# Kernel optimization log

Hardware: AMD Instinct MI355X
Metric: run time of the kernel (lower is better)

The kernel has to match this reference:

```python
import jax, jax.numpy as jnp
from jax import lax
import numpy as np

N_VOX = 50000
B = 2
D, H, W = 8, 160, 160
CIN = 16
G = 3
K = 27
CHANS = [(16, 16), (16, 32), (32, 64), (64, 64), (64, 128)]
NAMES = ['in', 'e1', 'e2', 'e3', 'out']


def setup_inputs() -> dict:
    key = jax.random.key(0)
    ks = jax.random.split(key, 16)
    rng = np.random.default_rng(0)
    # unique active cells -> deterministic scatter/gather rulebook
    lin = rng.choice(B * D * H * W, size=N_VOX, replace=False)
    bz = lin // (D * H * W)
    rem = lin % (D * H * W)
    zz = rem // (H * W)
    yy = (rem % (H * W)) // W
    xx = rem % W
    coors = jnp.asarray(np.stack([bz, zz, yy, xx], 1).astype(np.int32))
    inp = {
        'voxel_features': jax.random.normal(ks[0], (N_VOX, CIN), jnp.float32),
        'coors': coors,
        'batch_size': B,
    }
    i = 1
    for nm, (ci, co) in zip(NAMES, CHANS):
        k1, k2 = jax.random.split(ks[i]); i += 1
        inp['wb_' + nm] = jax.random.normal(k1, (K, ci, co), jnp.float32) * 0.05
        inp['ws_' + nm] = jax.random.normal(k2, (K, ci, G, co), jnp.float32) * 0.05
        inp['gm_' + nm] = jnp.ones((co,), jnp.float32)
        inp['bt_' + nm] = jnp.zeros((co,), jnp.float32)
    return inp


def _kan_block(feat, nbr, wb, ws, gm, bt, centers, inv_h):
    # submanifold KAN conv: gather -> (silu base + RBF spline basis) GEMM -> accumulate
    n = feat.shape[0]
    fp = jnp.concatenate([feat, jnp.zeros((1, feat.shape[1]), feat.dtype)], 0)  # pad row for out-of-grid

    def body(acc, kin):
        idx, wbk, wsk = kin
        x = fp[idx]                                   # [N, Cin] gathered neighbors
        base = jax.nn.silu(x) @ wbk                   # [N, Cout]
        bas = jnp.exp(-jnp.square((x[:, :, None] - centers) * inv_h))  # [N, Cin, G]
        spl = jnp.einsum('ncg,cgo->no', bas, wsk)     # [N, Cout]
        return acc + base + spl, None

    out0 = jnp.zeros((n, wb.shape[-1]), feat.dtype)
    out, _ = lax.scan(jax.checkpoint(body), out0, (nbr, wb, ws))
    # BatchNorm1d (train-mode batch stats) + ReLU
    mu = out.mean(0)
    var = out.var(0)
    out = (out - mu) * lax.rsqrt(var + 1e-3) * gm + bt
    return jax.nn.relu(out)


def _build_rulebook(coors, batch_size, n):
    grid = jnp.full((batch_size, D + 2, H + 2, W + 2), n, jnp.int32)
    grid = grid.at[coors[:, 0], coors[:, 1] + 1, coors[:, 2] + 1, coors[:, 3] + 1].set(
        jnp.arange(n, dtype=jnp.int32))
    offs = [(dz, dy, dx) for dz in (-1, 0, 1) for dy in (-1, 0, 1) for dx in (-1, 0, 1)]
    return jnp.stack([
        grid[coors[:, 0], coors[:, 1] + 1 + dz, coors[:, 2] + 1 + dy, coors[:, 3] + 1 + dx]
        for dz, dy, dx in offs])  # [27, N]


def reference(voxel_features, coors, batch_size,
              wb_in, ws_in, gm_in, bt_in,
              wb_e1, ws_e1, gm_e1, bt_e1,
              wb_e2, ws_e2, gm_e2, bt_e2,
              wb_e3, ws_e3, gm_e3, bt_e3,
              wb_out, ws_out, gm_out, bt_out):
    n = voxel_features.shape[0]
    nbr = _build_rulebook(coors, batch_size, n)
    centers = jnp.linspace(-1.0, 1.0, G)
    inv_h = (G - 1) / 2.0
    x = _kan_block(voxel_features, nbr, wb_in, ws_in, gm_in, bt_in, centers, inv_h)
    x = _kan_block(x, nbr, wb_e1, ws_e1, gm_e1, bt_e1, centers, inv_h)
    x = _kan_block(x, nbr, wb_e2, ws_e2, gm_e2, bt_e2, centers, inv_h)
    x = _kan_block(x, nbr, wb_e3, ws_e3, gm_e3, bt_e3, centers, inv_h)
    x = _kan_block(x, nbr, wb_out, ws_out, gm_out, bt_out, centers, inv_h)
    co = x.shape[1]
    dense = jnp.zeros((batch_size, D, H, W, co), x.dtype)
    dense = dense.at[coors[:, 0], coors[:, 1], coors[:, 2], coors[:, 3]].set(x)
    dense = dense.transpose(0, 4, 1, 2, 3)            # [B, C, D, H, W]
    return dense.reshape(batch_size, co * D, H, W)    # [B, C*D, H, W]
```

## Files before the change

### kernel.cpp

```cpp
#include <hip/hip_runtime.h>

#define N_VOX 50000
#define BATCH 2
#define DD 8
#define HH 160
#define WW 160
#define PD 10
#define PH 162
#define PW 162
#define KK 27
#define NCELL (BATCH*DD*HH*WW)
#define GRID_ELEMS (BATCH*PD*PH*PW)
#define OUT_ELEMS (BATCH*128*DD*HH*WW)

typedef __attribute__((ext_vector_type(8))) short short8v;
typedef __attribute__((ext_vector_type(4))) float float4v;

__device__ inline unsigned short f2bf(float f) {
    unsigned u = __float_as_uint(f);
    u += 0x7FFFu + ((u >> 16) & 1u);
    return (unsigned short)(u >> 16);
}

__global__ void k_flags(const int* __restrict__ coors, int* __restrict__ flags) {
    int n = blockIdx.x * 256 + threadIdx.x;
    if (n >= N_VOX) return;
    int b = coors[n*4+0], z = coors[n*4+1], y = coors[n*4+2], x = coors[n*4+3];
    flags[((b*DD + z)*HH + y)*WW + x] = 1;
}

__global__ void k_scan1(const int* __restrict__ flags, int* __restrict__ scanout,
                        int* __restrict__ bsums) {
    __shared__ int s[256];
    int t = threadIdx.x, blk = blockIdx.x;
    int4 v = ((const int4*)(flags + blk*1024))[t];
    int tsum = v.x + v.y + v.z + v.w;
    s[t] = tsum; __syncthreads();
    for (int off = 1; off < 256; off <<= 1) {
        int x = (t >= off) ? s[t-off] : 0;
        __syncthreads(); s[t] += x; __syncthreads();
    }
    int excl = s[t] - tsum;
    int4 o; o.x = excl; o.y = excl + v.x; o.z = o.y + v.y; o.w = o.z + v.z;
    ((int4*)(scanout + blk*1024))[t] = o;
    if (t == 255) bsums[blk] = s[255];
}

__global__ void k_scan2(int* __restrict__ bsums) {
    __shared__ int s[512];
    int t = threadIdx.x;
    int orig = (t < 400) ? bsums[t] : 0;
    s[t] = orig; __syncthreads();
    for (int off = 1; off < 512; off <<= 1) {
        int x = (t >= off) ? s[t-off] : 0;
        __syncthreads(); s[t] += x; __syncthreads();
    }
    if (t < 400) bsums[t] = s[t] - orig;
}

__global__ void k_pos(const int* __restrict__ coors, const int* __restrict__ scanout,
                      const int* __restrict__ bsums, int* __restrict__ pos_of,
                      int* __restrict__ vox_at) {
    int n = blockIdx.x * 256 + threadIdx.x;
    if (n >= N_VOX) return;
    int b = coors[n*4+0], z = coors[n*4+1], y = coors[n*4+2], x = coors[n*4+3];
    int lin = ((b*DD + z)*HH + y)*WW + x;
    int pos = scanout[lin] + bsums[lin >> 10];
    pos_of[n] = pos;
    vox_at[pos] = n;
}

__global__ void k_gridP(const int* __restrict__ coors, const int* __restrict__ pos_of,
                        int* __restrict__ gridP) {
    int n = blockIdx.x * 256 + threadIdx.x;
    if (n >= N_VOX) return;
    int b = coors[n*4+0], z = coors[n*4+1], y = coors[n*4+2], x = coors[n*4+3];
    gridP[((b*PD + z+1)*PH + (y+1))*PW + (x+1)] = pos_of[n];
}

__global__ void k_nbrP(const int* __restrict__ coors, const int* __restrict__ vox_at,
                       const int* __restrict__ gridP, int* __restrict__ nbrP) {
    int i = blockIdx.x * 256 + threadIdx.x;
    if (i >= N_VOX) return;
    int n = vox_at[i];
    int b = coors[n*4+0], z = coors[n*4+1]+1, y = coors[n*4+2]+1, x = coors[n*4+3]+1;
    int k = 0;
    for (int dz = -1; dz <= 1; ++dz)
        for (int dy = -1; dy <= 1; ++dy)
            for (int dx = -1; dx <= 1; ++dx) {
                int g = gridP[((b*PD + z+dz)*PH + (y+dy))*PW + (x+dx)];
                nbrP[k*N_VOX + i] = (g >= 0) ? g : N_VOX;
                ++k;
            }
}

__global__ void k_phi0(const float* __restrict__ vf, const int* __restrict__ vox_at,
                       unsigned short* __restrict__ phi) {
    int e = blockIdx.x * 256 + threadIdx.x;
    if (e >= (N_VOX + 1) * 16) return;
    int i = e / 16, c = e % 16;
    float x = 0.f;
    if (i < N_VOX) x = vf[(size_t)vox_at[i] * 16 + c];
    float sig = 1.f / (1.f + __expf(-x));
    ushort4 p;
    p.x = f2bf(x * sig);
    p.y = f2bf(__expf(-(x + 1.f) * (x + 1.f)));
    p.z = f2bf(__expf(-x * x));
    p.w = f2bf(__expf(-(x - 1.f) * (x - 1.f)));
    *(ushort4*)&phi[(size_t)e * 4] = p;
}

struct WswzArgs {
    const float* wb[5];
    const float* ws[5];
    unsigned short* dst[5];
};
__global__ void k_wswz_all(WswzArgs a) {
    constexpr int off[6]   = {0, 27648, 82944, 304128, 746496, 1631232};
    constexpr int lgCI4[5] = {6, 6, 7, 8, 8};
    constexpr int lgCO[5]  = {4, 5, 6, 6, 7};
    int e = blockIdx.x * 256 + threadIdx.x;
    if (e >= off[5]) return;
    int L = 0;
    #pragma unroll
    for (int i = 1; i < 5; ++i) L += (e >= off[i]);
    int el = e - off[L];
    int CIN4 = 1 << lgCI4[L], COUT = 1 << lgCO[L], CIN = CIN4 >> 2;
    int j8   = el & 7;
    int rest = el >> 3;
    int o    = rest & (COUT - 1);
    int kb   = rest >> lgCO[L];
    int kabs = kb * 8 + j8;
    int k  = kabs >> lgCI4[L];
    int c4 = kabs & (CIN4 - 1);
    int c = c4 >> 2, jj = c4 & 3;
    float v = (jj == 0) ? a.wb[L][(k * CIN + c) * COUT + o]
                        : a.ws[L][((k * CIN + c) * 3 + (jj - 1)) * COUT + o];
    a.dst[L][el] = f2bf(v);
}

template<int CIN, int COUT, int NSPL>
__global__ __launch_bounds__(256) void k_conv_mfma(
    const unsigned short* __restrict__ phi,
    const int*            __restrict__ nbrP,
    const unsigned short* __restrict__ Wsw,
    float*                __restrict__ pre,
    float*                __restrict__ sums)
{
    constexpr int CIN4   = CIN * 4;
    constexpr int BK     = 64;
    constexpr int SPK    = CIN4 / BK;
    constexpr int NSTAGE = KK * SPK;
    constexpr int COUTH  = COUT / NSPL;
    constexpr int NFW    = COUTH / 16;
    constexpr int NMB    = (N_VOX + 127) / 128;
    constexpr int NBLK   = NMB * NSPL;
    constexpr int PERX   = (NBLK + 7) / 8;

    int lb = blockIdx.x;
    int linear = (lb & 7) * PERX + (lb >> 3);
    if (linear >= NBLK) return;
    const int mb = linear / NSPL, h = linear % NSPL;

    const int t = threadIdx.x, lane = t & 63, wv = t >> 6;
    const int l15 = lane & 15, q = lane >> 4;
    const int base = mb * 128;
    const int vg0 = base + wv * 32 + l15, vg1 = vg0 + 16;
    const int ob = h * COUTH;

    const unsigned short* bp = Wsw + (size_t)(q * COUT + ob + l15) * 8;

    int rows[2], rowsN[2];
    short8v A0[2][2], A1[2][2];
    short8v B0[2][NFW], B1[2][NFW];

    auto loadB = [&](int sp, short8v (&Bb)[2][NFW]) {
        #pragma unroll
        for (int kk = 0; kk < 2; ++kk)
            #pragma unroll
            for (int nf = 0; nf < NFW; ++nf)
                Bb[kk][nf] = *(const short8v*)(bp +
                    ((size_t)(sp * 8 + kk * 4) * COUT + nf * 16) * 8);
    };
    auto loadA = [&](int sp, short8v (&Ab)[2][2]) {
        if (sp % SPK == 0) { rows[0] = rowsN[0]; rows[1] = rowsN[1]; }
        const int c4s = (sp % SPK) * BK;
        const unsigned short* p0 = phi + (size_t)rows[0] * CIN4 + c4s + q * 8;
        const unsigned short* p1 = phi + (size_t)rows[1] * CIN4 + c4s + q * 8;
        Ab[0][0] = *(const short8v*)p0;        Ab[0][1] = *(const short8v*)p1;
        Ab[1][0] = *(const short8v*)(p0 + 32); Ab[1][1] = *(const short8v*)(p1 + 32);
        if (sp % SPK == 0) {
            int k2 = sp / SPK + 1;
            if (k2 < KK) {
                rowsN[0] = (vg0 < N_VOX) ? nbrP[k2 * N_VOX + vg0] : N_VOX;
                rowsN[1] = (vg1 < N_VOX) ? nbrP[k2 * N_VOX + vg1] : N_VOX;
            }
        }
    };

    float4v acc[2][NFW];
    #pragma unroll
    for (int mi = 0; mi < 2; ++mi)
        #pragma unroll
        for (int nf = 0; nf < NFW; ++nf)
            acc[mi][nf] = (float4v){0.f, 0.f, 0.f, 0.f};

    auto domfma = [&](const short8v (&Ab)[2][2], const short8v (&Bb)[2][NFW]) {
        #pragma unroll
        for (int kk = 0; kk < 2; ++kk)
            #pragma unroll
            for (int nf = 0; nf < NFW; ++nf) {
                acc[0][nf] = __builtin_amdgcn_mfma_f32_16x16x32_bf16(Ab[kk][0], Bb[kk][nf], acc[0][nf], 0, 0, 0);
                acc[1][nf] = __builtin_amdgcn_mfma_f32_16x16x32_bf16(Ab[kk][1], Bb[kk][nf], acc[1][nf], 0, 0, 0);
            }
    };

    rows[0]  = (vg0 < N_VOX) ? nbrP[vg0] : N_VOX;
    rows[1]  = (vg1 < N_VOX) ? nbrP[vg1] : N_VOX;
    rowsN[0] = (vg0 < N_VOX) ? nbrP[N_VOX + vg0] : N_VOX;
    rowsN[1] = (vg1 < N_VOX) ? nbrP[N_VOX + vg1] : N_VOX;
    loadB(0, B0);
    {
        const unsigned short* p0 = phi + (size_t)rows[0] * CIN4 + q * 8;
        const unsigned short* p1 = phi + (size_t)rows[1] * CIN4 + q * 8;
        A0[0][0] = *(const short8v*)p0;        A0[0][1] = *(const short8v*)p1;
        A0[1][0] = *(const short8v*)(p0 + 32); A0[1][1] = *(const short8v*)(p1 + 32);
    }

    int s = 0;
    for (; s + 2 <= NSTAGE; s += 2) {
        loadB(s + 1, B1); loadA(s + 1, A1);
        __builtin_amdgcn_sched_barrier(0);
        domfma(A0, B0);
        if (s + 2 < NSTAGE) { loadB(s + 2, B0); loadA(s + 2, A0); }
        __builtin_amdgcn_sched_barrier(0);
        domfma(A1, B1);
    }
    if (s < NSTAGE) domfma(A0, B0);

    #pragma unroll
    for (int mi = 0; mi < 2; ++mi)
        #pragma unroll
        for (int nf = 0; nf < NFW; ++nf)
            #pragma unroll
            for (int r = 0; r < 4; ++r) {
                int v = base + wv * 32 + mi * 16 + q * 4 + r;
                if (v < N_VOX)
                    pre[(size_t)v * COUT + ob + nf * 16 + l15] = acc[mi][nf][r];
            }

    float* S = sums + (blockIdx.x & 7) * 256;
    #pragma unroll
    for (int nf = 0; nf < NFW; ++nf) {
        float s1 = 0.f, s2 = 0.f;
        #pragma unroll
        for (int mi = 0; mi < 2; ++mi)
            #pragma unroll
            for (int r = 0; r < 4; ++r) {
                int v = base + wv * 32 + mi * 16 + q * 4 + r;
                if (v < N_VOX) {
                    float a = acc[mi][nf][r];
                    s1 += a; s2 += a * a;
                }
            }
        s1 += __shfl_xor(s1, 16); s1 += __shfl_xor(s1, 32);
        s2 += __shfl_xor(s2, 16); s2 += __shfl_xor(s2, 32);
        if (q == 0) {
            atomicAdd(&S[ob + nf * 16 + l15], s1);
            atomicAdd(&S[COUT + ob + nf * 16 + l15], s2);
        }
    }
}

template<int COUT>
__global__ void k_bnapply_phi(const float* __restrict__ pre, const float* __restrict__ sums,
                              const float* __restrict__ gm, const float* __restrict__ bt,
                              unsigned short* __restrict__ phi) {
    __shared__ float sc[COUT], sh[COUT];
    int t = threadIdx.x;
    if (t < COUT) {
        float s1 = 0.f, s2 = 0.f;
        #pragma unroll
        for (int xo = 0; xo < 8; ++xo) {
            s1 += sums[xo * 256 + t];
            s2 += sums[xo * 256 + COUT + t];
        }
        float mu  = s1 * (1.f / N_VOX);
        float var = s2 * (1.f / N_VOX) - mu*mu;
        float s = rsqrtf(var + 1e-3f) * gm[t];
        sc[t] = s;
        sh[t] = bt[t] - mu * s;
    }
    __syncthreads();
    int tot = (N_VOX + 1) * COUT;
    for (int e = blockIdx.x*256 + t; e < tot; e += gridDim.x*256) {
        int i = e / COUT, c = e % COUT;
        float x = 0.f;
        if (i < N_VOX) x = fmaxf(pre[(size_t)i*COUT + c] * sc[c] + sh[c], 0.f);
        float sig = 1.f / (1.f + __expf(-x));
        ushort4 p;
        p.x = f2bf(x * sig);
        p.y = f2bf(__expf(-(x + 1.f) * (x + 1.f)));
        p.z = f2bf(__expf(-x * x));
        p.w = f2bf(__expf(-(x - 1.f) * (x - 1.f)));
        *(ushort4*)&phi[(size_t)e * 4] = p;
    }
}

template<int COUT>
__global__ void k_bnapply_f32(float* __restrict__ pre, const float* __restrict__ sums,
                              const float* __restrict__ gm, const float* __restrict__ bt) {
    __shared__ float sc[COUT], sh[COUT];
    int t = threadIdx.x;
    if (t < COUT) {
        float s1 = 0.f, s2 = 0.f;
        #pragma unroll
        for (int xo = 0; xo < 8; ++xo) {
            s1 += sums[xo * 256 + t];
            s2 += sums[xo * 256 + COUT + t];
        }
        float mu  = s1 * (1.f / N_VOX);
        float var = s2 * (1.f / N_VOX) - mu*mu;
        float s = rsqrtf(var + 1e-3f) * gm[t];
        sc[t] = s;
        sh[t] = bt[t] - mu * s;
    }
    __syncthreads();
    for (int e = blockIdx.x*256 + t; e < N_VOX*COUT; e += gridDim.x*256) {
        int c = e % COUT;
        pre[e] = fmaxf(pre[e] * sc[c] + sh[c], 0.f);
    }
}

__global__ void k_dense(const float* __restrict__ feat, const int* __restrict__ gridP,
                        float* __restrict__ out) {
    int e4 = blockIdx.x*256 + threadIdx.x;
    if (e4 >= OUT_ELEMS/4) return;
    int e = e4 * 4;
    int x  = e % WW;
    int y  = (e / WW) % HH;
    int cz = (e / (WW*HH)) % (128*DD);
    int b  = e / (WW*HH*128*DD);
    int c = cz >> 3, z = cz & 7;
    const int* gp = &gridP[((b*PD + z+1)*PH + (y+1))*PW + (x+1)];
    int g0 = gp[0], g1 = gp[1], g2 = gp[2], g3 = gp[3];
    float4 o;
    o.x = (g0 >= 0) ? feat[(size_t)g0*128 + c] : 0.f;
    o.y = (g1 >= 0) ? feat[(size_t)g1*128 + c] : 0.f;
    o.z = (g2 >= 0) ? feat[(size_t)g2*128 + c] : 0.f;
    o.w = (g3 >= 0) ? feat[(size_t)g3*128 + c] : 0.f;
    *(float4*)&out[e] = o;
}

template<int CIN, int COUT, int NSPL>
static void run_block(const float* gm, const float* bt,
                      const int* nbrP, unsigned short* phi, const unsigned short* Wsw,
                      float* sums, float* pre, bool last, hipStream_t stream) {
    constexpr int NMB  = (N_VOX + 127) / 128;
    constexpr int NBLK = NMB * NSPL;
    constexpr int GRID = ((NBLK + 7) / 8) * 8;
    k_conv_mfma<CIN, COUT, NSPL><<<GRID, 256, 0, stream>>>(phi, nbrP, Wsw, pre, sums);
    if (last) {
        k_bnapply_f32<COUT><<<512, 256, 0, stream>>>(pre, sums, gm, bt);
    } else {
        k_bnapply_phi<COUT><<<512, 256, 0, stream>>>(pre, sums, gm, bt, phi);
    }
}

extern "C" void kernel_launch(void* const* d_in, const int* in_sizes, int n_in,
                              void* d_out, int out_size, void* d_ws, size_t ws_size,
                              hipStream_t stream) {
    const float* vf    = (const float*)d_in[0];
    const int*   coors = (const int*)d_in[1];
    const float* wb[5] = {(const float*)d_in[3],  (const float*)d_in[7],
                          (const float*)d_in[11], (const float*)d_in[15],
                          (const float*)d_in[19]};
    const float* wsp[5]= {(const float*)d_in[4],  (const float*)d_in[8],
                          (const float*)d_in[12], (const float*)d_in[16],
                          (const float*)d_in[20]};
    const float* gm[5] = {(const float*)d_in[5],  (const float*)d_in[9],
                          (const float*)d_in[13], (const float*)d_in[17],
                          (const float*)d_in[21]};
    const float* bt[5] = {(const float*)d_in[6],  (const float*)d_in[10],
                          (const float*)d_in[14], (const float*)d_in[18],
                          (const float*)d_in[22]};

    char* p = (char*)d_ws;
    auto alloc = [&](size_t bytes) {
        char* r = p;
        p += (bytes + 255) & ~(size_t)255;
        return r;
    };
    int*            flags   = (int*)           alloc((size_t)NCELL * 4);
    int*            scanout = (int*)           alloc((size_t)NCELL * 4);
    int*            bsums   = (int*)           alloc(512 * 4);
    int*            pos_of  = (int*)           alloc((size_t)N_VOX * 4);
    int*            vox_at  = (int*)           alloc((size_t)N_VOX * 4);
    int*            gridP   = (int*)           alloc((size_t)GRID_ELEMS * 4);
    int*            nbrP    = (int*)           alloc((size_t)KK * N_VOX * 4);
    unsigned short* Wsw0    = (unsigned short*)alloc((size_t)KK * 64  * 16  * 2);
    unsigned short* Wsw1    = (unsigned short*)alloc((size_t)KK * 64  * 32  * 2);
    unsigned short* Wsw2    = (unsigned short*)alloc((size_t)KK * 128 * 64  * 2);
    unsigned short* Wsw3    = (unsigned short*)alloc((size_t)KK * 256 * 64  * 2);
    unsigned short* Wsw4    = (unsigned short*)alloc((size_t)KK * 256 * 128 * 2);
    unsigned short* phi     = (unsigned short*)alloc((size_t)(N_VOX + 1) * 256 * 2);
    float*          sumsAll = (float*)         alloc(5 * 8 * 256 * 4);
    float*          pre     = (float*)         alloc((size_t)N_VOX * 128 * 4);

    hipMemsetAsync(flags, 0, (size_t)NCELL * 4, stream);
    hipMemsetAsync(gridP, 0xFF, (size_t)GRID_ELEMS * 4, stream);
    hipMemsetAsync(sumsAll, 0, 5 * 8 * 256 * 4, stream);

    WswzArgs wa;
    for (int i = 0; i < 5; ++i) { wa.wb[i] = wb[i]; wa.ws[i] = wsp[i]; }
    wa.dst[0] = Wsw0; wa.dst[1] = Wsw1; wa.dst[2] = Wsw2; wa.dst[3] = Wsw3; wa.dst[4] = Wsw4;
    k_wswz_all<<<(1631232 + 255) / 256, 256, 0, stream>>>(wa);

    k_flags<<<(N_VOX+255)/256, 256, 0, stream>>>(coors, flags);
    k_scan1<<<NCELL/1024, 256, 0, stream>>>(flags, scanout, bsums);
    k_scan2<<<1, 512, 0, stream>>>(bsums);
    k_pos  <<<(N_VOX+255)/256, 256, 0, stream>>>(coors, scanout, bsums, pos_of, vox_at);
    k_gridP<<<(N_VOX+255)/256, 256, 0, stream>>>(coors, pos_of, gridP);
    k_nbrP <<<(N_VOX+255)/256, 256, 0, stream>>>(coors, vox_at, gridP, nbrP);
    {
        int n = (N_VOX + 1) * 16;
        k_phi0<<<(n + 255) / 256, 256, 0, stream>>>(vf, vox_at, phi);
    }

    run_block<16, 16,  1>(gm[0], bt[0], nbrP, phi, Wsw0, sumsAll + 0*2048, pre, false, stream);
    run_block<16, 32,  1>(gm[1], bt[1], nbrP, phi, Wsw1, sumsAll + 1*2048, pre, false, stream);
    run_block<32, 64,  1>(gm[2], bt[2], nbrP, phi, Wsw2, sumsAll + 2*2048, pre, false, stream);
    run_block<64, 64,  1>(gm[3], bt[3], nbrP, phi, Wsw3, sumsAll + 3*2048, pre, false, stream);
    run_block<64, 128, 2>(gm[4], bt[4], nbrP, phi, Wsw4, sumsAll + 4*2048, pre, true,  stream);

    k_dense<<<(OUT_ELEMS/4 + 255)/256, 256, 0, stream>>>(pre, gridP, (float*)d_out);
}
```

Baseline: 737.9 us.

## Use 32x32x16 bf16 MFMA for conv layers with COUT>=32

Adds a conv kernel built on the 32x32x16 bf16 MFMA. It is used for layers 1-4, while layer 0 (COUT=16) keeps the 16x16 variant. The weight swizzle kernel now emits a matching 16-element-per-output layout for those layers. The aim is fewer MFMA instructions and better operand reuse per gathered A row, since one wave covers 32 voxels in a single tile. In exchange each lane holds more accumulator registers (16 floats per output tile), which may reduce occupancy.

```diff
diff --git a/kernel.cpp b/kernel.cpp
--- a/kernel.cpp
+++ b/kernel.cpp
@@ -13,8 +13,9 @@
 #define GRID_ELEMS (BATCH*PD*PH*PW)
 #define OUT_ELEMS (BATCH*128*DD*HH*WW)
 
-typedef __attribute__((ext_vector_type(8))) short short8v;
-typedef __attribute__((ext_vector_type(4))) float float4v;
+typedef __attribute__((ext_vector_type(8)))  short short8v;
+typedef __attribute__((ext_vector_type(4)))  float float4v;
+typedef __attribute__((ext_vector_type(16))) float float16v;
 
 __device__ inline unsigned short f2bf(float f) {
     unsigned u = __float_as_uint(f);
@@ -126,11 +127,20 @@
     for (int i = 1; i < 5; ++i) L += (e >= off[i]);
     int el = e - off[L];
     int CIN4 = 1 << lgCI4[L], COUT = 1 << lgCO[L], CIN = CIN4 >> 2;
-    int j8   = el & 7;
-    int rest = el >> 3;
-    int o    = rest & (COUT - 1);
-    int kb   = rest >> lgCO[L];
-    int kabs = kb * 8 + j8;
+    int kabs, o;
+    if (L == 0) {
+        int j8 = el & 7;
+        int rest = el >> 3;
+        o = rest & (COUT - 1);
+        int kb = rest >> lgCO[L];
+        kabs = kb * 8 + j8;
+    } else {
+        int j = el & 7;
+        int half = (el >> 3) & 1;
+        o = (el >> 4) & (COUT - 1);
+        int kb = el >> (4 + lgCO[L]);
+        kabs = kb * 16 + half * 8 + j;
+    }
     int k  = kabs >> lgCI4[L];
     int c4 = kabs & (CIN4 - 1);
     int c = c4 >> 2, jj = c4 & 3;
@@ -139,36 +149,32 @@
     a.dst[L][el] = f2bf(v);
 }
 
-template<int CIN, int COUT, int NSPL>
-__global__ __launch_bounds__(256) void k_conv_mfma(
-    const unsigned short* __restrict__ phi,
-    const int*            __restrict__ nbrP,
-    const unsigned short* __restrict__ Wsw,
-    float*                __restrict__ pre,
-    float*                __restrict__ sums)
+template<int CIN, int COUT>
+__global__ __launch_bounds__(256) void k_conv_mfma16(
+    const unsigned short* __restrict__ phi, const int* __restrict__ nbrP,
+    const unsigned short* __restrict__ Wsw, float* __restrict__ pre,
+    float* __restrict__ sums)
 {
     constexpr int CIN4   = CIN * 4;
     constexpr int BK     = 64;
     constexpr int SPK    = CIN4 / BK;
     constexpr int NSTAGE = KK * SPK;
-    constexpr int COUTH  = COUT / NSPL;
-    constexpr int NFW    = COUTH / 16;
+    constexpr int NFW    = COUT / 16;
     constexpr int NMB    = (N_VOX + 127) / 128;
-    constexpr int NBLK   = NMB * NSPL;
+    constexpr int NBLK   = NMB;
     constexpr int PERX   = (NBLK + 7) / 8;
 
     int lb = blockIdx.x;
     int linear = (lb & 7) * PERX + (lb >> 3);
     if (linear >= NBLK) return;
-    const int mb = linear / NSPL, h = linear % NSPL;
+    const int mb = linear;
 
     const int t = threadIdx.x, lane = t & 63, wv = t >> 6;
     const int l15 = lane & 15, q = lane >> 4;
     const int base = mb * 128;
     const int vg0 = base + wv * 32 + l15, vg1 = vg0 + 16;
-    const int ob = h * COUTH;
-
-    const unsigned short* bp = Wsw + (size_t)(q * COUT + ob + l15) * 8;
+
+    const unsigned short* bp = Wsw + (size_t)(q * COUT + l15) * 8;
 
     int rows[2], rowsN[2];
     short8v A0[2][2], A1[2][2];
@@ -246,7 +252,7 @@
             for (int r = 0; r < 4; ++r) {
                 int v = base + wv * 32 + mi * 16 + q * 4 + r;
                 if (v < N_VOX)
-                    pre[(size_t)v * COUT + ob + nf * 16 + l15] = acc[mi][nf][r];
+                    pre[(size_t)v * COUT + nf * 16 + l15] = acc[mi][nf][r];
             }
 
     float* S = sums + (blockIdx.x & 7) * 256;
@@ -266,8 +272,131 @@
         s1 += __shfl_xor(s1, 16); s1 += __shfl_xor(s1, 32);
         s2 += __shfl_xor(s2, 16); s2 += __shfl_xor(s2, 32);
         if (q == 0) {
-            atomicAdd(&S[ob + nf * 16 + l15], s1);
-            atomicAdd(&S[COUT + ob + nf * 16 + l15], s2);
+            atomicAdd(&S[nf * 16 + l15], s1);
+            atomicAdd(&S[COUT + nf * 16 + l15], s2);
+        }
+    }
+}
+
+template<int CIN, int COUT, int NSPL>
+__global__ __launch_bounds__(256) void k_conv_mfma32(
+    const unsigned short* __restrict__ phi,
+    const int*            __restrict__ nbrP,
+    const unsigned short* __restrict__ Wsw,
+    float*                __restrict__ pre,
+    float*                __restrict__ sums)
+{
+    constexpr int CIN4   = CIN * 4;
+    constexpr int BK     = 64;
+    constexpr int SPK    = CIN4 / BK;
+    constexpr int NSTAGE = KK * SPK;
+    constexpr int COUTH  = COUT / NSPL;
+    constexpr int NF     = COUTH / 32;
+    constexpr int NMB    = (N_VOX + 127) / 128;
+    constexpr int NBLK   = NMB * NSPL;
+    constexpr int PERX   = (NBLK + 7) / 8;
+
+    int lb = blockIdx.x;
+    int linear = (lb & 7) * PERX + (lb >> 3);
+    if (linear >= NBLK) return;
+    const int mb = linear / NSPL, h = linear % NSPL;
+
+    const int t = threadIdx.x, lane = t & 63, wv = t >> 6;
+    const int l31 = lane & 31, half = lane >> 5;
+    const int base = mb * 128;
+    const int vg = base + wv * 32 + l31;
+    const int ob = h * COUTH;
+
+    const unsigned short* bp = Wsw + (size_t)((ob + l31) * 2 + half) * 8;
+
+    int row, rowN;
+    short8v A0[4], A1[4];
+    short8v B0[4][NF], B1[4][NF];
+
+    auto loadB = [&](int sp, short8v (&Bb)[4][NF]) {
+        #pragma unroll
+        for (int ks = 0; ks < 4; ++ks)
+            #pragma unroll
+            for (int nf = 0; nf < NF; ++nf)
+                Bb[ks][nf] = *(const short8v*)(bp +
+                    (size_t)((sp * 4 + ks) * COUT + nf * 32) * 16);
+    };
+    auto loadA = [&](int sp, short8v (&Ab)[4]) {
+        if (sp % SPK == 0) row = rowN;
+        const int c4s = (sp % SPK) * BK;
+        const unsigned short* p = phi + (size_t)row * CIN4 + c4s + half * 8;
+        #pragma unroll
+        for (int ks = 0; ks < 4; ++ks)
+            Ab[ks] = *(const short8v*)(p + ks * 16);
+        if (sp % SPK == 0) {
+            int k2 = sp / SPK + 1;
+            if (k2 < KK) rowN = (vg < N_VOX) ? nbrP[k2 * N_VOX + vg] : N_VOX;
+        }
+    };
+
+    float16v acc[NF];
+    #pragma unroll
+    for (int nf = 0; nf < NF; ++nf)
+        #pragma unroll
+        for (int r = 0; r < 16; ++r) acc[nf][r] = 0.f;
+
+    auto domfma = [&](const short8v (&Ab)[4], const short8v (&Bb)[4][NF]) {
+        #pragma unroll
+        for (int ks = 0; ks < 4; ++ks)
+            #pragma unroll
+            for (int nf = 0; nf < NF; ++nf)
+                acc[nf] = __builtin_amdgcn_mfma_f32_32x32x16_bf16(Ab[ks], Bb[ks][nf], acc[nf], 0, 0, 0);
+    };
+
+    row  = (vg < N_VOX) ? nbrP[vg] : N_VOX;
+    rowN = (vg < N_VOX) ? nbrP[N_VOX + vg] : N_VOX;
+    loadB(0, B0);
+    {
+        const unsigned short* p = phi + (size_t)row * CIN4 + half * 8;
+        #pragma unroll
+        for (int ks = 0; ks < 4; ++ks)
+            A0[ks] = *(const short8v*)(p + ks * 16);
+    }
+
+    int s = 0;
+    for (; s + 2 <= NSTAGE; s += 2) {
+        loadB(s + 1, B1); loadA(s + 1, A1);
+        __builtin_amdgcn_sched_barrier(0);
+        domfma(A0, B0);
+        if (s + 2 < NSTAGE) { loadB(s + 2, B0); loadA(s + 2, A0); }
+        __builtin_amdgcn_sched_barrier(0);
+        domfma(A1, B1);
+    }
+    if (s < NSTAGE) domfma(A0, B0);
+
+    #pragma unroll
+    for (int nf = 0; nf < NF; ++nf)
+        #pragma unroll
+        for (int r = 0; r < 16; ++r) {
+            int rw = (r & 3) + 8 * (r >> 2) + 4 * half;
+            int v = base + wv * 32 + rw;
+            if (v < N_VOX)
+                pre[(size_t)v * COUT + ob + nf * 32 + l31] = acc[nf][r];
+        }
+
+    float* S = sums + (blockIdx.x & 7) * 256;
+    #pragma unroll
+    for (int nf = 0; nf < NF; ++nf) {
+        float s1 = 0.f, s2 = 0.f;
+        #pragma unroll
+        for (int r = 0; r < 16; ++r) {
+            int rw = (r & 3) + 8 * (r >> 2) + 4 * half;
+            int v = base + wv * 32 + rw;
+            if (v < N_VOX) {
+                float a = acc[nf][r];
+                s1 += a; s2 += a * a;
+            }
+        }
+        s1 += __shfl_xor(s1, 32);
+        s2 += __shfl_xor(s2, 32);
+        if (half == 0) {
+            atomicAdd(&S[ob + nf * 32 + l31], s1);
+            atomicAdd(&S[COUT + ob + nf * 32 + l31], s2);
         }
     }
 }
@@ -353,13 +482,13 @@
 }
 
 template<int CIN, int COUT, int NSPL>
-static void run_block(const float* gm, const float* bt,
-                      const int* nbrP, unsigned short* phi, const unsigned short* Wsw,
-                      float* sums, float* pre, bool last, hipStream_t stream) {
+static void run_block32(const float* gm, const float* bt,
+                        const int* nbrP, unsigned short* phi, const unsigned short* Wsw,
+                        float* sums, float* pre, bool last, hipStream_t stream) {
     constexpr int NMB  = (N_VOX + 127) / 128;
     constexpr int NBLK = NMB * NSPL;
     constexpr int GRID = ((NBLK + 7) / 8) * 8;
-    k_conv_mfma<CIN, COUT, NSPL><<<GRID, 256, 0, stream>>>(phi, nbrP, Wsw, pre, sums);
+    k_conv_mfma32<CIN, COUT, NSPL><<<GRID, 256, 0, stream>>>(phi, nbrP, Wsw, pre, sums);
     if (last) {
         k_bnapply_f32<COUT><<<512, 256, 0, stream>>>(pre, sums, gm, bt);
     } else {
@@ -427,11 +556,17 @@
         k_phi0<<<(n + 255) / 256, 256, 0, stream>>>(vf, vox_at, phi);
     }
 
-    run_block<16, 16,  1>(gm[0], bt[0], nbrP, phi, Wsw0, sumsAll + 0*2048, pre, false, stream);
-    run_block<16, 32,  1>(gm[1], bt[1], nbrP, phi, Wsw1, sumsAll + 1*2048, pre, false, stream);
-    run_block<32, 64,  1>(gm[2], bt[2], nbrP, phi, Wsw2, sumsAll + 2*2048, pre, false, stream);
-    run_block<64, 64,  1>(gm[3], bt[3], nbrP, phi, Wsw3, sumsAll + 3*2048, pre, false, stream);
-    run_block<64, 128, 2>(gm[4], bt[4], nbrP, phi, Wsw4, sumsAll + 4*2048, pre, true,  stream);
+    {
+        constexpr int NMB = (N_VOX + 127) / 128;
+        constexpr int GRID = ((NMB + 7) / 8) * 8;
+        k_conv_mfma16<16, 16><<<GRID, 256, 0, stream>>>(phi, nbrP, Wsw0, pre, sumsAll + 0*2048);
+        k_bnapply_phi<16><<<512, 256, 0, stream>>>(pre, sumsAll + 0*2048, gm[0], bt[0], phi);
+    }
+
+    run_block32<16, 32,  1>(gm[1], bt[1], nbrP, phi, Wsw1, sumsAll + 1*2048, pre, false, stream);
+    run_block32<32, 64,  1>(gm[2], bt[2], nbrP, phi, Wsw2, sumsAll + 2*2048, pre, false, stream);
+    run_block32<64, 64,  1>(gm[3], bt[3], nbrP, phi, Wsw3, sumsAll + 3*2048, pre, false, stream);
+    run_block32<64, 128, 2>(gm[4], bt[4], nbrP, phi, Wsw4, sumsAll + 4*2048, pre, true,  stream);
 
     k_dense<<<(OUT_ELEMS/4 + 255)/256, 256, 0, stream>>>(pre, gridP, (float*)d_out);
 }
```

Result: no change. 750.6 us (+1.7%).

## Stage conv weights through double-buffered LDS shared by all waves

Applied to the files above, without the earlier changes.

Adds a new conv kernel in which the block cooperatively loads weight tiles for groups of three stages into double-buffered shared memory, instead of each wave fetching its B fragments from global memory into registers. The four waves then read B from LDS while the gathered activation rows are still prefetched per stage. The aim is to cut redundant global and L2 weight traffic and register pressure across waves. The cost is a __syncthreads per group and LDS usage that may limit occupancy. The first layer keeps the old register-path kernel, now specialised without the output-channel split.

```diff
diff --git a/kernel.cpp b/kernel.cpp
--- a/kernel.cpp
+++ b/kernel.cpp
@@ -139,36 +139,32 @@
     a.dst[L][el] = f2bf(v);
 }
 
-template<int CIN, int COUT, int NSPL>
-__global__ __launch_bounds__(256) void k_conv_mfma(
-    const unsigned short* __restrict__ phi,
-    const int*            __restrict__ nbrP,
-    const unsigned short* __restrict__ Wsw,
-    float*                __restrict__ pre,
-    float*                __restrict__ sums)
+template<int CIN, int COUT>
+__global__ __launch_bounds__(256) void k_conv_mfma16(
+    const unsigned short* __restrict__ phi, const int* __restrict__ nbrP,
+    const unsigned short* __restrict__ Wsw, float* __restrict__ pre,
+    float* __restrict__ sums)
 {
     constexpr int CIN4   = CIN * 4;
     constexpr int BK     = 64;
     constexpr int SPK    = CIN4 / BK;
     constexpr int NSTAGE = KK * SPK;
-    constexpr int COUTH  = COUT / NSPL;
-    constexpr int NFW    = COUTH / 16;
+    constexpr int NFW    = COUT / 16;
     constexpr int NMB    = (N_VOX + 127) / 128;
-    constexpr int NBLK   = NMB * NSPL;
+    constexpr int NBLK   = NMB;
     constexpr int PERX   = (NBLK + 7) / 8;
 
     int lb = blockIdx.x;
     int linear = (lb & 7) * PERX + (lb >> 3);
     if (linear >= NBLK) return;
-    const int mb = linear / NSPL, h = linear % NSPL;
+    const int mb = linear;
 
     const int t = threadIdx.x, lane = t & 63, wv = t >> 6;
     const int l15 = lane & 15, q = lane >> 4;
     const int base = mb * 128;
     const int vg0 = base + wv * 32 + l15, vg1 = vg0 + 16;
-    const int ob = h * COUTH;
-
-    const unsigned short* bp = Wsw + (size_t)(q * COUT + ob + l15) * 8;
+
+    const unsigned short* bp = Wsw + (size_t)(q * COUT + l15) * 8;
 
     int rows[2], rowsN[2];
     short8v A0[2][2], A1[2][2];
@@ -237,6 +233,157 @@
         domfma(A1, B1);
     }
     if (s < NSTAGE) domfma(A0, B0);
+
+    #pragma unroll
+    for (int mi = 0; mi < 2; ++mi)
+        #pragma unroll
+        for (int nf = 0; nf < NFW; ++nf)
+            #pragma unroll
+            for (int r = 0; r < 4; ++r) {
+                int v = base + wv * 32 + mi * 16 + q * 4 + r;
+                if (v < N_VOX)
+                    pre[(size_t)v * COUT + nf * 16 + l15] = acc[mi][nf][r];
+            }
+
+    float* S = sums + (blockIdx.x & 7) * 256;
+    #pragma unroll
+    for (int nf = 0; nf < NFW; ++nf) {
+        float s1 = 0.f, s2 = 0.f;
+        #pragma unroll
+        for (int mi = 0; mi < 2; ++mi)
+            #pragma unroll
+            for (int r = 0; r < 4; ++r) {
+                int v = base + wv * 32 + mi * 16 + q * 4 + r;
+                if (v < N_VOX) {
+                    float a = acc[mi][nf][r];
+                    s1 += a; s2 += a * a;
+                }
+            }
+        s1 += __shfl_xor(s1, 16); s1 += __shfl_xor(s1, 32);
+        s2 += __shfl_xor(s2, 16); s2 += __shfl_xor(s2, 32);
+        if (q == 0) {
+            atomicAdd(&S[nf * 16 + l15], s1);
+            atomicAdd(&S[COUT + nf * 16 + l15], s2);
+        }
+    }
+}
+
+template<int CIN, int COUT, int NSPL, int G>
+__global__ __launch_bounds__(256) void k_conv_lds(
+    const unsigned short* __restrict__ phi,
+    const int*            __restrict__ nbrP,
+    const unsigned short* __restrict__ Wsw,
+    float*                __restrict__ pre,
+    float*                __restrict__ sums)
+{
+    constexpr int CIN4   = CIN * 4;
+    constexpr int BK     = 64;
+    constexpr int SPK    = CIN4 / BK;
+    constexpr int NSTAGE = KK * SPK;
+    constexpr int NG     = NSTAGE / G;
+    constexpr int COUTH  = COUT / NSPL;
+    constexpr int NFW    = COUTH / 16;
+    constexpr int NMB    = (N_VOX + 127) / 128;
+    constexpr int NBLK   = NMB * NSPL;
+    constexpr int PERX   = (NBLK + 7) / 8;
+    constexpr int GCH    = G * 8 * COUTH;
+    constexpr int NLD    = GCH / 256;
+
+    __shared__ short Bs[2][G * 8 * COUTH * 8];
+
+    int lb = blockIdx.x;
+    int linear = (lb & 7) * PERX + (lb >> 3);
+    if (linear >= NBLK) return;
+    const int mb = linear / NSPL, h = linear % NSPL;
+
+    const int t = threadIdx.x, lane = t & 63, wv = t >> 6;
+    const int l15 = lane & 15, q = lane >> 4;
+    const int base = mb * 128;
+    const int vg0 = base + wv * 32 + l15, vg1 = vg0 + 16;
+    const int ob = h * COUTH;
+
+    uint4 sreg[NLD];
+    const uint4* wsrc = (const uint4*)Wsw;
+    auto sload = [&](int gr) {
+        #pragma unroll
+        for (int i = 0; i < NLD; ++i) {
+            int c = t + i * 256;
+            int kbl = c / COUTH, oo = c % COUTH;
+            sreg[i] = wsrc[(size_t)(gr * G * 8 + kbl) * COUT + ob + oo];
+        }
+    };
+    auto swrite = [&](int buf) {
+        uint4* dst = (uint4*)&Bs[buf][0];
+        #pragma unroll
+        for (int i = 0; i < NLD; ++i) dst[t + i * 256] = sreg[i];
+    };
+
+    int rows[2], rowsN[2];
+    short8v A[2][2], An[2][2];
+    auto loadA = [&](int sp, short8v (&Ab)[2][2]) {
+        if (sp % SPK == 0) { rows[0] = rowsN[0]; rows[1] = rowsN[1]; }
+        const int c4s = (sp % SPK) * BK;
+        const unsigned short* p0 = phi + (size_t)rows[0] * CIN4 + c4s + q * 8;
+        const unsigned short* p1 = phi + (size_t)rows[1] * CIN4 + c4s + q * 8;
+        Ab[0][0] = *(const short8v*)p0;        Ab[0][1] = *(const short8v*)p1;
+        Ab[1][0] = *(const short8v*)(p0 + 32); Ab[1][1] = *(const short8v*)(p1 + 32);
+        if (sp % SPK == 0) {
+            int k2 = sp / SPK + 1;
+            if (k2 < KK) {
+                rowsN[0] = (vg0 < N_VOX) ? nbrP[k2 * N_VOX + vg0] : N_VOX;
+                rowsN[1] = (vg1 < N_VOX) ? nbrP[k2 * N_VOX + vg1] : N_VOX;
+            }
+        }
+    };
+
+    rows[0]  = (vg0 < N_VOX) ? nbrP[vg0] : N_VOX;
+    rows[1]  = (vg1 < N_VOX) ? nbrP[vg1] : N_VOX;
+    rowsN[0] = (vg0 < N_VOX) ? nbrP[N_VOX + vg0] : N_VOX;
+    rowsN[1] = (vg1 < N_VOX) ? nbrP[N_VOX + vg1] : N_VOX;
+    {
+        const unsigned short* p0 = phi + (size_t)rows[0] * CIN4 + q * 8;
+        const unsigned short* p1 = phi + (size_t)rows[1] * CIN4 + q * 8;
+        A[0][0] = *(const short8v*)p0;        A[0][1] = *(const short8v*)p1;
+        A[1][0] = *(const short8v*)(p0 + 32); A[1][1] = *(const short8v*)(p1 + 32);
+    }
+    sload(0);
+    swrite(0);
+    __syncthreads();
+
+    float4v acc[2][NFW];
+    #pragma unroll
+    for (int mi = 0; mi < 2; ++mi)
+        #pragma unroll
+        for (int nf = 0; nf < NFW; ++nf)
+            acc[mi][nf] = (float4v){0.f, 0.f, 0.f, 0.f};
+
+    int buf = 0;
+    for (int gr = 0; gr < NG; ++gr) {
+        if (gr + 1 < NG) sload(gr + 1);
+        const short* bb = &Bs[buf][0];
+        #pragma unroll
+        for (int ls = 0; ls < G; ++ls) {
+            const int s = gr * G + ls;
+            const bool pf = (s + 1 < NSTAGE);
+            if (pf) loadA(s + 1, An);
+            #pragma unroll
+            for (int kk = 0; kk < 2; ++kk)
+                #pragma unroll
+                for (int nf = 0; nf < NFW; ++nf) {
+                    short8v bfr = *(const short8v*)(bb +
+                        ((size_t)((ls * 8 + kk * 4 + q) * COUTH) + nf * 16 + l15) * 8);
+                    acc[0][nf] = __builtin_amdgcn_mfma_f32_16x16x32_bf16(A[kk][0], bfr, acc[0][nf], 0, 0, 0);
+                    acc[1][nf] = __builtin_amdgcn_mfma_f32_16x16x32_bf16(A[kk][1], bfr, acc[1][nf], 0, 0, 0);
+                }
+            if (pf) {
+                #pragma unroll
+                for (int kk = 0; kk < 2; ++kk) { A[kk][0] = An[kk][0]; A[kk][1] = An[kk][1]; }
+            }
+        }
+        if (gr + 1 < NG) swrite(buf ^ 1);
+        __syncthreads();
+        buf ^= 1;
+    }
 
     #pragma unroll
     for (int mi = 0; mi < 2; ++mi)
@@ -359,7 +506,7 @@
     constexpr int NMB  = (N_VOX + 127) / 128;
     constexpr int NBLK = NMB * NSPL;
     constexpr int GRID = ((NBLK + 7) / 8) * 8;
-    k_conv_mfma<CIN, COUT, NSPL><<<GRID, 256, 0, stream>>>(phi, nbrP, Wsw, pre, sums);
+    k_conv_lds<CIN, COUT, NSPL, 3><<<GRID, 256, 0, stream>>>(phi, nbrP, Wsw, pre, sums);
     if (last) {
         k_bnapply_f32<COUT><<<512, 256, 0, stream>>>(pre, sums, gm, bt);
     } else {
@@ -427,7 +574,13 @@
         k_phi0<<<(n + 255) / 256, 256, 0, stream>>>(vf, vox_at, phi);
     }
 
-    run_block<16, 16,  1>(gm[0], bt[0], nbrP, phi, Wsw0, sumsAll + 0*2048, pre, false, stream);
+    {
+        constexpr int NMB = (N_VOX + 127) / 128;
+        constexpr int GRID = ((NMB + 7) / 8) * 8;
+        k_conv_mfma16<16, 16><<<GRID, 256, 0, stream>>>(phi, nbrP, Wsw0, pre, sumsAll + 0*2048);
+        k_bnapply_phi<16><<<512, 256, 0, stream>>>(pre, sumsAll + 0*2048, gm[0], bt[0], phi);
+    }
+
     run_block<16, 32,  1>(gm[1], bt[1], nbrP, phi, Wsw1, sumsAll + 1*2048, pre, false, stream);
     run_block<32, 64,  1>(gm[2], bt[2], nbrP, phi, Wsw2, sumsAll + 2*2048, pre, false, stream);
     run_block<64, 64,  1>(gm[3], bt[3], nbrP, phi, Wsw3, sumsAll + 3*2048, pre, false, stream);
```

Measured after the change: 962.7 us. 1.3x slower.
